# Kernel tuning notes

Measured on AMD Instinct MI355X. Metric: run time of the kernel, lower is better.

Reference implementation:

```python
import jax, jax.numpy as jnp
import numpy as np

B = 8          # batch size (static)
GRID = 1024    # spatial grid H = W
PER = 25000    # active sites per batch item
N = B * PER

_OFFSETS = [(dx, dy) for dx in (-1, 0, 1) for dy in (-1, 0, 1)]  # 3x3 kernel


def _build_sparse_inputs():
    """Sample unique active 2D coords per batch item and build the 3x3
    submanifold neighbor map: nbr[i, k] = index of neighbor site at kernel
    offset k, or -1 if that coordinate is inactive."""
    rng = np.random.default_rng(0)
    bs, xs, ys = [], [], []
    for b in range(B):
        flat = rng.choice(GRID * GRID, size=PER, replace=False)
        bs.append(np.full(PER, b, np.int64))
        xs.append((flat // GRID).astype(np.int64))
        ys.append((flat % GRID).astype(np.int64))
    bb = np.concatenate(bs); xx = np.concatenate(xs); yy = np.concatenate(ys)
    # hash lookup table: (b, x, y) -> site index
    lut = np.full(B * GRID * GRID, -1, np.int64)
    lut[bb * GRID * GRID + xx * GRID + yy] = np.arange(N, dtype=np.int64)
    nbr = np.full((N, 9), -1, np.int64)
    for k, (dx, dy) in enumerate(_OFFSETS):
        nx, ny = xx + dx, yy + dy
        ok = (nx >= 0) & (nx < GRID) & (ny >= 0) & (ny < GRID)
        key = bb * GRID * GRID + np.clip(nx, 0, GRID - 1) * GRID + np.clip(ny, 0, GRID - 1)
        nbr[:, k] = np.where(ok, lut[key], -1)
    return bb, nbr


def setup_inputs() -> dict:
    key = jax.random.key(0)
    k1, k2, k3 = jax.random.split(key, 3)
    batch_np, nbr_np = _build_sparse_inputs()
    feats = jax.random.normal(k1, (N, 3), dtype=jnp.float32)
    # He (kaiming normal, relu): std = sqrt(2 / fan_in), fan_in = 9 * Cin
    W1 = jax.random.normal(k2, (9, 3, 256), dtype=jnp.float32) * np.sqrt(2.0 / (9 * 3))
    W2 = jax.random.normal(k3, (9, 256, 256), dtype=jnp.float32) * np.sqrt(2.0 / (9 * 256))
    return {
        "feats": feats,
        "W1": W1,
        "W2": W2,
        "nbr": jnp.asarray(nbr_np),
        "batch_ids": jnp.asarray(batch_np),
    }


def _subm_conv(feat, W, nbr):
    """Submanifold 3x3 conv: out[i] = sum_k feat[nbr[i,k]] @ W[k] over valid
    neighbors. feat: [N, Cin], W: [9, Cin, Cout], nbr: [N, 9] -> [N, Cout]."""
    out = jnp.zeros((feat.shape[0], W.shape[2]), dtype=feat.dtype)
    for k in range(9):  # fixed small kernel loop
        idx = nbr[:, k]
        valid = (idx >= 0).astype(feat.dtype)[:, None]
        g = feat[jnp.maximum(idx, 0)] * valid  # masked gather [N, Cin]
        out = out + g @ W[k]
    return out


def reference(feats, W1, W2, nbr, batch_ids):
    h = jax.nn.relu(_subm_conv(feats, W1, nbr))   # [N, 256]
    h = jax.nn.relu(_subm_conv(h, W2, nbr))       # [N, 256]
    # global average pool per batch item -> [B, 256]
    sums = jax.ops.segment_sum(h, batch_ids, num_segments=B)
    counts = jax.ops.segment_sum(jnp.ones((h.shape[0],), h.dtype), batch_ids, num_segments=B)
    return sums / counts[:, None]
```

## Files before the change

### kernel.cpp

```cpp
#include <hip/hip_runtime.h>
#include <hip/hip_bf16.h>

typedef __attribute__((ext_vector_type(8))) short bh8;
typedef __attribute__((ext_vector_type(4))) float f32x4;

#define NB 8
#define SLOTS 64
#define CAP 6144
#define CROWS 36864
#define CGB 256
#define FROWS 64

__device__ __forceinline__ void gld_lds16(const void* g, void* l) {
  __builtin_amdgcn_global_load_lds(
      (const __attribute__((address_space(1))) void*)g,
      (__attribute__((address_space(3))) void*)l, 16, 0, 0);
}

__device__ __forceinline__ unsigned short f2bu(float f) {
  union { __hip_bfloat16 h; unsigned short u; } cv;
  cv.h = __float2bfloat16(f);
  return cv.u;
}
__device__ __forceinline__ float bu2f(unsigned short u) {
  return __uint_as_float(((unsigned)u) << 16);
}

__global__ __launch_bounds__(256, 2) void phase1_kernel(
    const float* __restrict__ feats, const float* __restrict__ W1,
    const float* __restrict__ W2, const int* __restrict__ nbr,
    const int* __restrict__ bid, __hip_bfloat16* __restrict__ h1b,
    __hip_bfloat16* __restrict__ w2bt, int* __restrict__ nOff,
    int* __restrict__ cnt, float* __restrict__ bcnt, int* __restrict__ cidmap,
    int* __restrict__ crow, int* __restrict__ psrc, int* __restrict__ pcnt_cid,
    int* __restrict__ pairlist, int N) {
  __shared__ union {
    struct { unsigned short w1s[256 * 32]; int s_nbr[64 * 9]; } c1;
    struct { int l_cnt[10]; int l_base[10]; int l_bcnt[NB]; } bld;
    struct { float tile[16][256]; } w2;
  } sm;

  const int nc1 = (N + 63) >> 6;
  const int nbld = (N + 255) >> 8;
  int bx = blockIdx.x;
  const int tid = threadIdx.x;

  if (bx < nc1) {
    const int base = bx * 64;
#pragma unroll 9
    for (int kk = 0; kk < 27; ++kk)
      sm.c1.w1s[tid * 32 + kk] = f2bu(W1[kk * 256 + tid]);
#pragma unroll
    for (int kk = 27; kk < 32; ++kk) sm.c1.w1s[tid * 32 + kk] = 0;
    for (int t = tid; t < 64 * 9; t += 256) sm.c1.s_nbr[t] = nbr[base * 9 + t];
    __syncthreads();

    const int wave = tid >> 6, lane = tid & 63;
    const int q = lane >> 4, m16 = lane & 15;
    const int rbase = (wave * 16 + m16) * 9;
    const int* s_nbr = sm.c1.s_nbr;

    float v[9 * 3];
    int t_lo[4] = {0, 2, 5, 8}, t_hi[4] = {3, 6, 8, 9};
    for (int tt = t_lo[q]; tt < t_hi[q]; ++tt) {
      int s = s_nbr[rbase + tt];
      long long sc = (s < 0) ? 0 : s;
      float x = feats[3 * sc], y = feats[3 * sc + 1], z = feats[3 * sc + 2];
      if (s < 0) { x = 0.f; y = 0.f; z = 0.f; }
      v[tt * 3 + 0] = x; v[tt * 3 + 1] = y; v[tt * 3 + 2] = z;
    }
    bh8 a;
#pragma unroll
    for (int j = 0; j < 8; ++j) {
      int col = q * 8 + j;
      a[j] = (col < 27) ? (short)f2bu(v[col]) : (short)0;
    }

    f32x4 acc[16];
#pragma unroll
    for (int nj = 0; nj < 16; ++nj) {
      bh8 b = *(const bh8*)(&sm.c1.w1s[(nj * 16 + m16) * 32 + q * 8]);
      acc[nj] = __builtin_amdgcn_mfma_f32_16x16x32_bf16(a, b, (f32x4)0.f, 0, 0, 0);
    }
    const int growb = base + wave * 16 + q * 4;
#pragma unroll
    for (int rr = 0; rr < 4; ++rr) {
      __hip_bfloat16* rowp = h1b + (long long)(growb + rr) * 256 + m16;
#pragma unroll
      for (int nj = 0; nj < 16; ++nj)
        rowp[nj * 16] = __float2bfloat16(fmaxf(acc[nj][rr], 0.f));
    }
    return;
  }
  bx -= nc1;

  if (bx < nbld) {
    if (tid < 10) sm.bld.l_cnt[tid] = 0;
    if (tid < NB) sm.bld.l_bcnt[tid] = 0;
    __syncthreads();

    const int i = bx * 256 + tid;
    const bool active = (i < N);
    int s[9];
    int kpos[9];
    int loc_cid = -1;
    if (active) {
#pragma unroll
      for (int k = 0; k < 9; ++k) s[k] = nbr[i * 9 + k];
      bool any = false;
#pragma unroll
      for (int k = 0; k < 9; ++k)
        if (k != 4 && s[k] >= 0) any = true;
      if (any) {
        loc_cid = atomicAdd(&sm.bld.l_cnt[9], 1);
#pragma unroll
        for (int k = 0; k < 9; ++k) {
          kpos[k] = -1;
          if (k != 4 && s[k] >= 0) kpos[k] = atomicAdd(&sm.bld.l_cnt[k], 1);
        }
      }
      atomicAdd(&sm.bld.l_bcnt[bid[i]], 1);
    }
    __syncthreads();

    if (tid < 9)
      sm.bld.l_base[tid] =
          (sm.bld.l_cnt[tid] > 0) ? atomicAdd(&cnt[tid], sm.bld.l_cnt[tid]) : 0;
    else if (tid == 9)
      sm.bld.l_base[9] = (sm.bld.l_cnt[9] > 0) ? atomicAdd(nOff, sm.bld.l_cnt[9]) : 0;
    if (tid >= 32 && tid < 32 + NB && sm.bld.l_bcnt[tid - 32] > 0)
      atomicAdd(&bcnt[tid - 32], (float)sm.bld.l_bcnt[tid - 32]);
    __syncthreads();

    if (active) {
      int cid = -1;
      if (loc_cid >= 0) {
        cid = sm.bld.l_base[9] + loc_cid;
        if (cid >= CROWS) cid = -1;
      }
      cidmap[i] = cid;
      if (cid >= 0) {
        crow[cid] = i;
#pragma unroll
        for (int k = 0; k < 9; ++k) {
          if (k == 4 || kpos[k] < 0 || s[k] < 0) continue;
          int pos = sm.bld.l_base[k] + kpos[k];
          if (pos < CAP) {
            psrc[k * CAP + pos] = s[k];
            int slot = atomicAdd(&pcnt_cid[cid], 1);
            if (slot < 8) pairlist[cid * 8 + slot] = k * CAP + pos;
          }
        }
      }
    }
    return;
  }
  bx -= nbld;

  {
    int k = bx >> 4, t = bx & 15;
#pragma unroll
    for (int r = 0; r < 16; ++r)
      sm.w2.tile[r][tid] = W2[k * 65536 + (t * 16 + r) * 256 + tid];
    __syncthreads();
#pragma unroll
    for (int r = 0; r < 16; ++r)
      w2bt[k * 65536 + tid * 256 + t * 16 + r] = __float2bfloat16(sm.w2.tile[r][tid]);
  }
}

__global__ __launch_bounds__(512, 2) void phase2_kernel(
    const __hip_bfloat16* __restrict__ h1, const __hip_bfloat16* __restrict__ w2bt,
    const int* __restrict__ cidmap, const int* __restrict__ bid,
    const int* __restrict__ cnt, const int* __restrict__ psrc,
    const int* __restrict__ nOffp, const int* __restrict__ crow,
    float* __restrict__ psums, unsigned short* __restrict__ h2cb,
    unsigned short* __restrict__ pout, int N) {
  __shared__ __align__(16) short Abuf[2][64 * 256];

  int bx = blockIdx.x;
  const int tid = threadIdx.x;
  const int wave = tid >> 6, lane = tid & 63;
  const int q = lane >> 4, m16 = lane & 15;
  const short* h1s = (const short*)h1;

  if (bx < CGB) {
    const int wc = wave << 5;
    const int slot = bx & (SLOTS - 1);
    const short* wts = (const short*)w2bt + 4 * 65536;

    bh8 breg[2][8];
#pragma unroll
    for (int nj = 0; nj < 2; ++nj)
#pragma unroll
      for (int ko = 0; ko < 8; ++ko)
        breg[nj][ko] =
            *(const bh8*)(wts + (wc + nj * 16 + m16) * 256 + ko * 32 + q * 8);

    const int nchunk = (N + 63) >> 6;
    const int span = (nchunk + CGB - 1) / CGB;
    const int c0 = bx * span;
    if (c0 >= nchunk) return;
    int c1 = c0 + span;
    if (c1 > nchunk) c1 = nchunk;

    const int lrow = lane >> 5;
    const int jch = lane & 31;

#define STAGE_CHUNK(cc, b)                                                     \
  {                                                                            \
    _Pragma("unroll") for (int t = 0; t < 4; ++t) {                            \
      int lr = (wave << 3) + (t << 1) + lrow;                                  \
      int g = ((cc) << 6) + lr;                                                \
      if (g >= N) g = N - 1;                                                   \
      int js = jch ^ (lr & 31);                                                \
      const short* src = h1s + (long long)g * 256 + (js << 3);                 \
      short* dst = &Abuf[b][((wave << 3) + (t << 1)) << 8];                    \
      gld_lds16((const void*)src, (void*)dst);                                 \
    }                                                                          \
  }

#define FLUSH_SACC()                                                           \
  if (cur_b0 >= 0) {                                                           \
    _Pragma("unroll") for (int lb = 0; lb < 2; ++lb) {                         \
      _Pragma("unroll") for (int nj = 0; nj < 2; ++nj) {                       \
        float v = sacc[lb][nj];                                                \
        v += __shfl_xor(v, 16, 64);                                            \
        v += __shfl_xor(v, 32, 64);                                            \
        if (q == 0 && v != 0.f) {                                              \
          int b = cur_b0 + lb;                                                 \
          if (b < NB)                                                          \
            atomicAdd(&psums[(slot * NB + b) * 256 + wc + nj * 16 + m16], v);  \
        }                                                                      \
      }                                                                        \
    }                                                                          \
  }

    STAGE_CHUNK(c0, 0);
    int cur = 0;
    int cur_b0 = -1;
    float sacc[2][2];
#pragma unroll
    for (int lb = 0; lb < 2; ++lb)
#pragma unroll
      for (int nj = 0; nj < 2; ++nj) sacc[lb][nj] = 0.f;

    for (int c = c0; c < c1; ++c) {
      __syncthreads();

      int4 bid4[4], cid4[4];
#pragma unroll
      for (int mi = 0; mi < 4; ++mi) {
        const int rb = (c << 6) + mi * 16 + q * 4;
        bid4[mi] = *(const int4*)(&bid[rb]);
        cid4[mi] = *(const int4*)(&cidmap[rb]);
      }
      const int b0 = bid[c << 6];

      if (c + 1 < c1) STAGE_CHUNK(c + 1, cur ^ 1);

      const short* Ab = &Abuf[cur][0];
      const short* abase[4];
      int xr[4];
#pragma unroll
      for (int mi = 0; mi < 4; ++mi) {
        int R = mi * 16 + m16;
        xr[mi] = R & 31;
        abase[mi] = Ab + (R << 8);
      }

      f32x4 acc[4][2];
#pragma unroll
      for (int ko = 0; ko < 8; ++ko) {
        bh8 a[4];
#pragma unroll
        for (int mi = 0; mi < 4; ++mi)
          a[mi] = *(const bh8*)(abase[mi] + (((ko * 4 + q) ^ xr[mi]) << 3));
#pragma unroll
        for (int mi = 0; mi < 4; ++mi)
#pragma unroll
          for (int nj = 0; nj < 2; ++nj)
            acc[mi][nj] = __builtin_amdgcn_mfma_f32_16x16x32_bf16(
                a[mi], breg[nj][ko], (ko == 0) ? (f32x4)0.f : acc[mi][nj], 0, 0, 0);
      }

      if (b0 != cur_b0) {
        FLUSH_SACC();
#pragma unroll
        for (int lb = 0; lb < 2; ++lb)
#pragma unroll
          for (int nj = 0; nj < 2; ++nj) sacc[lb][nj] = 0.f;
        cur_b0 = b0;
      }
#pragma unroll
      for (int mi = 0; mi < 4; ++mi) {
        const int bb[4] = {bid4[mi].x, bid4[mi].y, bid4[mi].z, bid4[mi].w};
        const int cc4[4] = {cid4[mi].x, cid4[mi].y, cid4[mi].z, cid4[mi].w};
        const int rb = (c << 6) + mi * 16 + q * 4;
#pragma unroll
        for (int rr = 0; rr < 4; ++rr) {
          if (rb + rr >= N) continue;
          if (cc4[rr] >= 0) continue;
          const int lb = (bb[rr] != b0) ? 1 : 0;
#pragma unroll
          for (int nj = 0; nj < 2; ++nj)
            sacc[lb][nj] += fmaxf(acc[mi][nj][rr], 0.f);
        }
      }
      cur ^= 1;
    }
    FLUSH_SACC();
#undef STAGE_CHUNK
#undef FLUSH_SACC
    return;
  }
  bx -= CGB;

  int* s_src = (int*)&Abuf[0][0];
  const int OFFG = 8 * (CAP / 64);
  int k = 4;
  int gbase, cmax;
  bool isoff;
  if (bx < OFFG) {
    int koff = bx / (CAP / 64);
    int grp = bx - koff * (CAP / 64);
    k = koff + (koff >= 4 ? 1 : 0);
    cmax = cnt[k];
    gbase = grp * 64;
    isoff = true;
  } else {
    bx -= OFFG;
    cmax = *nOffp;
    if (cmax > CROWS) cmax = CROWS;
    gbase = bx * 64;
    isoff = false;
  }
  if (gbase >= cmax) return;

  if (tid < 64) {
    int m = gbase + tid;
    s_src[tid] = (m < cmax) ? (isoff ? psrc[k * CAP + m] : crow[m]) : 0;
  }
  const short* wts = (const short*)w2bt + k * 65536;
  const int wc = wave << 5;

  bh8 breg[2][8];
#pragma unroll
  for (int nj = 0; nj < 2; ++nj)
#pragma unroll
    for (int ko = 0; ko < 8; ++ko)
      breg[nj][ko] = *(const bh8*)(wts + (wc + nj * 16 + m16) * 256 + ko * 32 + q * 8);
  __syncthreads();

  for (int t = 0; t < 4; ++t) {
    if (gbase + t * 16 >= cmax) break;
    bh8 aA[8];
    {
      const short* ap = h1s + (long long)s_src[t * 16 + m16] * 256 + q * 8;
#pragma unroll
      for (int ko = 0; ko < 8; ++ko) aA[ko] = *(const bh8*)(ap + ko * 32);
    }
    f32x4 acc[2];
#pragma unroll
    for (int ko = 0; ko < 8; ++ko)
#pragma unroll
      for (int nj = 0; nj < 2; ++nj)
        acc[nj] = __builtin_amdgcn_mfma_f32_16x16x32_bf16(
            aA[ko], breg[nj][ko], (ko == 0) ? (f32x4)0.f : acc[nj], 0, 0, 0);
#pragma unroll
    for (int r = 0; r < 4; ++r) {
      int m = gbase + t * 16 + q * 4 + r;
      if (m >= cmax) continue;
      unsigned short* dst =
          isoff ? (pout + (long long)(k * CAP + m) * 256) : (h2cb + (long long)m * 256);
      dst[wc + m16] = f2bu(acc[0][r]);
      dst[wc + 16 + m16] = f2bu(acc[1][r]);
    }
  }
}

__global__ __launch_bounds__(256) void fixup_kernel(
    const unsigned short* __restrict__ h2cb, const unsigned short* __restrict__ pout,
    const int* __restrict__ pairlist, const int* __restrict__ pcnt_cid,
    const int* __restrict__ crow, const int* __restrict__ bid,
    const int* __restrict__ nOffp, float* __restrict__ psums) {
  __shared__ float lsum[NB * 256];
  __shared__ int s_b[FROWS], s_np[FROWS], s_pl[FROWS * 8];
  int nc = *nOffp;
  if (nc > CROWS) nc = CROWS;
  const int t0 = blockIdx.x * FROWS;
  if (t0 >= nc) return;
  const int tid = threadIdx.x;

  if (tid < FROWS) {
    int m = t0 + tid;
    bool v = (m < nc);
    s_b[tid] = v ? bid[crow[m]] : -1;
    int np = v ? pcnt_cid[m] : 0;
    s_np[tid] = (np > 8) ? 8 : np;
  }
  for (int i = tid; i < FROWS * 8; i += 256) {
    int m = t0 + (i >> 3);
    s_pl[i] = (m < nc) ? pairlist[m * 8 + (i & 7)] : 0;
  }
#pragma unroll
  for (int b = 0; b < NB; ++b) lsum[b * 256 + tid] = 0.f;
  __syncthreads();

  const int g = tid >> 6;
  const int cg = tid & 63;
  const ushort4* h2v = (const ushort4*)h2cb;
  const ushort4* pov = (const ushort4*)pout;

  float4 s0 = {0.f, 0.f, 0.f, 0.f}, s1 = {0.f, 0.f, 0.f, 0.f};
  const int r0 = g * 16;
  const int b0 = s_b[r0];
  int b1 = -1;
  for (int r = r0; r < r0 + 16; ++r) {
    const int b = s_b[r];
    if (b < 0) break;
    ushort4 u = h2v[(long long)(t0 + r) * 64 + cg];
    float4 x = {bu2f(u.x), bu2f(u.y), bu2f(u.z), bu2f(u.w)};
    const int np = s_np[r];
    for (int j = 0; j < np; ++j) {
      ushort4 p = pov[(long long)s_pl[r * 8 + j] * 64 + cg];
      x.x += bu2f(p.x); x.y += bu2f(p.y); x.z += bu2f(p.z); x.w += bu2f(p.w);
    }
    x.x = fmaxf(x.x, 0.f); x.y = fmaxf(x.y, 0.f);
    x.z = fmaxf(x.z, 0.f); x.w = fmaxf(x.w, 0.f);
    if (b == b0) {
      s0.x += x.x; s0.y += x.y; s0.z += x.z; s0.w += x.w;
    } else {
      b1 = b;
      s1.x += x.x; s1.y += x.y; s1.z += x.z; s1.w += x.w;
    }
  }
  if (b0 >= 0) {
    float* p0 = &lsum[b0 * 256 + cg * 4];
    atomicAdd(p0 + 0, s0.x); atomicAdd(p0 + 1, s0.y);
    atomicAdd(p0 + 2, s0.z); atomicAdd(p0 + 3, s0.w);
  }
  if (b1 >= 0 && b1 < NB) {
    float* p1 = &lsum[b1 * 256 + cg * 4];
    atomicAdd(p1 + 0, s1.x); atomicAdd(p1 + 1, s1.y);
    atomicAdd(p1 + 2, s1.z); atomicAdd(p1 + 3, s1.w);
  }
  __syncthreads();

  const int slot = blockIdx.x & (SLOTS - 1);
#pragma unroll
  for (int b = 0; b < NB; ++b) {
    float v = lsum[b * 256 + tid];
    if (v != 0.f) atomicAdd(&psums[(slot * NB + b) * 256 + tid], v);
  }
}

__global__ void finalize_kernel(const float* __restrict__ psums,
                                const float* __restrict__ bcnt,
                                float* __restrict__ out) {
  int b = blockIdx.x, c = threadIdx.x;
  float s = 0.f;
  for (int t = 0; t < SLOTS; ++t) s += psums[(t * NB + b) * 256 + c];
  out[b * 256 + c] = s / bcnt[b];
}

extern "C" void kernel_launch(void* const* d_in, const int* in_sizes, int n_in,
                              void* d_out, int out_size, void* d_ws, size_t ws_size,
                              hipStream_t stream) {
  const float* feats = (const float*)d_in[0];
  const float* W1    = (const float*)d_in[1];
  const float* W2    = (const float*)d_in[2];
  const int*   nbr   = (const int*)d_in[3];
  const int*   bid   = (const int*)d_in[4];
  float* out = (float*)d_out;
  const int N = in_sizes[0] / 3;

  char* ws = (char*)d_ws;
  size_t o = 0;
  float* psums = (float*)(ws + o); o += (size_t)SLOTS * NB * 256 * 4;
  float* bcnt  = (float*)(ws + o); o += NB * 4;
  int*   nOff  = (int*)(ws + o);   o += 4;
  int*   cnt   = (int*)(ws + o);   o += 9 * 4;
  o = (o + 255) & ~(size_t)255;
  int* pcnt_cid = (int*)(ws + o); o += (size_t)CROWS * 4;
  size_t zero1 = o;
  int* psrc = (int*)(ws + o); o += (size_t)9 * CAP * 4;
  int* pairlist = (int*)(ws + o); o += (size_t)CROWS * 8 * 4;
  int* cidmap = (int*)(ws + o); o += (size_t)N * 4;
  int* crow = (int*)(ws + o); o += (size_t)CROWS * 4;
  o = (o + 255) & ~(size_t)255;
  unsigned short* h2cb = (unsigned short*)(ws + o); o += (size_t)CROWS * 256 * 2;
  unsigned short* pout = (unsigned short*)(ws + o); o += (size_t)9 * CAP * 256 * 2;
  __hip_bfloat16* w2bt = (__hip_bfloat16*)(ws + o); o += (size_t)9 * 65536 * 2;
  __hip_bfloat16* h1b  = (__hip_bfloat16*)(ws + o); o += (size_t)N * 256 * 2;

  hipMemsetAsync(d_ws, 0, zero1, stream);

  const int nc1 = (N + 63) / 64;
  const int nbld = (N + 255) / 256;
  phase1_kernel<<<nc1 + nbld + 144, 256, 0, stream>>>(
      feats, W1, W2, nbr, bid, h1b, w2bt, nOff, cnt, bcnt, cidmap, crow, psrc,
      pcnt_cid, pairlist, N);
  phase2_kernel<<<CGB + 8 * (CAP / 64) + CROWS / 64, 512, 0, stream>>>(
      h1b, w2bt, cidmap, bid, cnt, psrc, nOff, crow, psums, h2cb, pout, N);
  fixup_kernel<<<(CROWS + FROWS - 1) / FROWS, 256, 0, stream>>>(
      h2cb, pout, pairlist, pcnt_cid, crow, bid, nOff, psums);
  finalize_kernel<<<NB, 256, 0, stream>>>(psums, bcnt, out);
}
```

Before: 272.1 us.

## Split phase2 into separate off-center and center GEMM kernels with prefetching

The merged phase2 kernel is split into two launches. One is an off-center/center-row gather GEMM kernel with 256 threads, where each wave covers 64 output columns and the next 16-row A tile is prefetched into registers. The other is a dedicated center-tap GEMM kernel that keeps the LDS double-buffered pipeline. The phase1 feature gather is also unrolled into explicit per-quarter branches to avoid a dynamic-indexed register array. The goal is to cut register/LDS pressure for the off-center blocks and give each kernel its own occupancy. The cost is an extra launch boundary and serialization between the two GEMMs.

```diff
diff --git a/kernel.cpp b/kernel.cpp
--- a/kernel.cpp
+++ b/kernel.cpp
@@ -8,7 +8,7 @@
 #define SLOTS 64
 #define CAP 6144
 #define CROWS 36864
-#define CGB 256
+#define CBLOCKS 256
 #define FROWS 64
 
 __device__ __forceinline__ void gld_lds16(const void* g, void* l) {
@@ -24,6 +24,16 @@
 }
 __device__ __forceinline__ float bu2f(unsigned short u) {
   return __uint_as_float(((unsigned)u) << 16);
+}
+
+__device__ __forceinline__ float3 ldf3(const float* __restrict__ f,
+                                       const int* s_nbr, int idx) {
+  int s = s_nbr[idx];
+  long long sc = (s < 0) ? 0 : s;
+  float3 r;
+  r.x = f[3 * sc]; r.y = f[3 * sc + 1]; r.z = f[3 * sc + 2];
+  if (s < 0) { r.x = 0.f; r.y = 0.f; r.z = 0.f; }
+  return r;
 }
 
 __global__ __launch_bounds__(256, 2) void phase1_kernel(
@@ -60,20 +70,34 @@
     const int rbase = (wave * 16 + m16) * 9;
     const int* s_nbr = sm.c1.s_nbr;
 
-    float v[9 * 3];
-    int t_lo[4] = {0, 2, 5, 8}, t_hi[4] = {3, 6, 8, 9};
-    for (int tt = t_lo[q]; tt < t_hi[q]; ++tt) {
-      int s = s_nbr[rbase + tt];
-      long long sc = (s < 0) ? 0 : s;
-      float x = feats[3 * sc], y = feats[3 * sc + 1], z = feats[3 * sc + 2];
-      if (s < 0) { x = 0.f; y = 0.f; z = 0.f; }
-      v[tt * 3 + 0] = x; v[tt * 3 + 1] = y; v[tt * 3 + 2] = z;
-    }
     bh8 a;
-#pragma unroll
-    for (int j = 0; j < 8; ++j) {
-      int col = q * 8 + j;
-      a[j] = (col < 27) ? (short)f2bu(v[col]) : (short)0;
+    if (q == 0) {
+      float3 t0 = ldf3(feats, s_nbr, rbase + 0);
+      float3 t1 = ldf3(feats, s_nbr, rbase + 1);
+      float3 t2 = ldf3(feats, s_nbr, rbase + 2);
+      a[0] = (short)f2bu(t0.x); a[1] = (short)f2bu(t0.y); a[2] = (short)f2bu(t0.z);
+      a[3] = (short)f2bu(t1.x); a[4] = (short)f2bu(t1.y); a[5] = (short)f2bu(t1.z);
+      a[6] = (short)f2bu(t2.x); a[7] = (short)f2bu(t2.y);
+    } else if (q == 1) {
+      float3 t2 = ldf3(feats, s_nbr, rbase + 2);
+      float3 t3 = ldf3(feats, s_nbr, rbase + 3);
+      float3 t4 = ldf3(feats, s_nbr, rbase + 4);
+      float3 t5 = ldf3(feats, s_nbr, rbase + 5);
+      a[0] = (short)f2bu(t2.z);
+      a[1] = (short)f2bu(t3.x); a[2] = (short)f2bu(t3.y); a[3] = (short)f2bu(t3.z);
+      a[4] = (short)f2bu(t4.x); a[5] = (short)f2bu(t4.y); a[6] = (short)f2bu(t4.z);
+      a[7] = (short)f2bu(t5.x);
+    } else if (q == 2) {
+      float3 t5 = ldf3(feats, s_nbr, rbase + 5);
+      float3 t6 = ldf3(feats, s_nbr, rbase + 6);
+      float3 t7 = ldf3(feats, s_nbr, rbase + 7);
+      a[0] = (short)f2bu(t5.y); a[1] = (short)f2bu(t5.z);
+      a[2] = (short)f2bu(t6.x); a[3] = (short)f2bu(t6.y); a[4] = (short)f2bu(t6.z);
+      a[5] = (short)f2bu(t7.x); a[6] = (short)f2bu(t7.y); a[7] = (short)f2bu(t7.z);
+    } else {
+      float3 t8 = ldf3(feats, s_nbr, rbase + 8);
+      a[0] = (short)f2bu(t8.x); a[1] = (short)f2bu(t8.y); a[2] = (short)f2bu(t8.z);
+      a[3] = 0; a[4] = 0; a[5] = 0; a[6] = 0; a[7] = 0;
     }
 
     f32x4 acc[16];
@@ -169,43 +193,37 @@
   }
 }
 
-__global__ __launch_bounds__(512, 2) void phase2_kernel(
+__global__ __launch_bounds__(512, 2) void center_gemm_kernel(
     const __hip_bfloat16* __restrict__ h1, const __hip_bfloat16* __restrict__ w2bt,
     const int* __restrict__ cidmap, const int* __restrict__ bid,
-    const int* __restrict__ cnt, const int* __restrict__ psrc,
-    const int* __restrict__ nOffp, const int* __restrict__ crow,
-    float* __restrict__ psums, unsigned short* __restrict__ h2cb,
-    unsigned short* __restrict__ pout, int N) {
+    float* __restrict__ psums, int N) {
   __shared__ __align__(16) short Abuf[2][64 * 256];
 
-  int bx = blockIdx.x;
   const int tid = threadIdx.x;
   const int wave = tid >> 6, lane = tid & 63;
   const int q = lane >> 4, m16 = lane & 15;
+  const int wc = wave << 5;
+  const int slot = blockIdx.x & (SLOTS - 1);
+
   const short* h1s = (const short*)h1;
-
-  if (bx < CGB) {
-    const int wc = wave << 5;
-    const int slot = bx & (SLOTS - 1);
-    const short* wts = (const short*)w2bt + 4 * 65536;
-
-    bh8 breg[2][8];
-#pragma unroll
-    for (int nj = 0; nj < 2; ++nj)
-#pragma unroll
-      for (int ko = 0; ko < 8; ++ko)
-        breg[nj][ko] =
-            *(const bh8*)(wts + (wc + nj * 16 + m16) * 256 + ko * 32 + q * 8);
-
-    const int nchunk = (N + 63) >> 6;
-    const int span = (nchunk + CGB - 1) / CGB;
-    const int c0 = bx * span;
-    if (c0 >= nchunk) return;
-    int c1 = c0 + span;
-    if (c1 > nchunk) c1 = nchunk;
-
-    const int lrow = lane >> 5;
-    const int jch = lane & 31;
+  const short* wts = (const short*)w2bt + 4 * 65536;
+
+  bh8 breg[2][8];
+#pragma unroll
+  for (int nj = 0; nj < 2; ++nj)
+#pragma unroll
+    for (int ko = 0; ko < 8; ++ko)
+      breg[nj][ko] = *(const bh8*)(wts + (wc + nj * 16 + m16) * 256 + ko * 32 + q * 8);
+
+  const int nchunk = (N + 63) >> 6;
+  const int span = (nchunk + CBLOCKS - 1) / CBLOCKS;
+  const int c0 = blockIdx.x * span;
+  if (c0 >= nchunk) return;
+  int c1 = c0 + span;
+  if (c1 > nchunk) c1 = nchunk;
+
+  const int lrow = lane >> 5;
+  const int jch = lane & 31;
 
 #define STAGE_CHUNK(cc, b)                                                     \
   {                                                                            \
@@ -236,100 +254,104 @@
     }                                                                          \
   }
 
-    STAGE_CHUNK(c0, 0);
-    int cur = 0;
-    int cur_b0 = -1;
-    float sacc[2][2];
-#pragma unroll
-    for (int lb = 0; lb < 2; ++lb)
-#pragma unroll
-      for (int nj = 0; nj < 2; ++nj) sacc[lb][nj] = 0.f;
-
-    for (int c = c0; c < c1; ++c) {
-      __syncthreads();
-
-      int4 bid4[4], cid4[4];
-#pragma unroll
-      for (int mi = 0; mi < 4; ++mi) {
-        const int rb = (c << 6) + mi * 16 + q * 4;
-        bid4[mi] = *(const int4*)(&bid[rb]);
-        cid4[mi] = *(const int4*)(&cidmap[rb]);
+  STAGE_CHUNK(c0, 0);
+  int cur = 0;
+  int cur_b0 = -1;
+  float sacc[2][2];
+#pragma unroll
+  for (int lb = 0; lb < 2; ++lb)
+#pragma unroll
+    for (int nj = 0; nj < 2; ++nj) sacc[lb][nj] = 0.f;
+
+  for (int c = c0; c < c1; ++c) {
+    __syncthreads();
+
+    int4 bid4[4], cid4[4];
+#pragma unroll
+    for (int mi = 0; mi < 4; ++mi) {
+      const int rb = (c << 6) + mi * 16 + q * 4;
+      bid4[mi] = *(const int4*)(&bid[rb]);
+      cid4[mi] = *(const int4*)(&cidmap[rb]);
+    }
+    const int b0 = bid[c << 6];
+
+    if (c + 1 < c1) STAGE_CHUNK(c + 1, cur ^ 1);
+
+    const short* Ab = &Abuf[cur][0];
+    const short* abase[4];
+    int xr[4];
+#pragma unroll
+    for (int mi = 0; mi < 4; ++mi) {
+      int R = mi * 16 + m16;
+      xr[mi] = R & 31;
+      abase[mi] = Ab + (R << 8);
+    }
+
+    f32x4 acc[4][2];
+#pragma unroll
+    for (int ko = 0; ko < 8; ++ko) {
+      bh8 a[4];
+#pragma unroll
+      for (int mi = 0; mi < 4; ++mi)
+        a[mi] = *(const bh8*)(abase[mi] + (((ko * 4 + q) ^ xr[mi]) << 3));
+#pragma unroll
+      for (int mi = 0; mi < 4; ++mi)
+#pragma unroll
+        for (int nj = 0; nj < 2; ++nj)
+          acc[mi][nj] = __builtin_amdgcn_mfma_f32_16x16x32_bf16(
+              a[mi], breg[nj][ko], (ko == 0) ? (f32x4)0.f : acc[mi][nj], 0, 0, 0);
+    }
+
+    if (b0 != cur_b0) {
+      FLUSH_SACC();
+#pragma unroll
+      for (int lb = 0; lb < 2; ++lb)
+#pragma unroll
+        for (int nj = 0; nj < 2; ++nj) sacc[lb][nj] = 0.f;
+      cur_b0 = b0;
+    }
+#pragma unroll
+    for (int mi = 0; mi < 4; ++mi) {
+      const int bb[4] = {bid4[mi].x, bid4[mi].y, bid4[mi].z, bid4[mi].w};
+      const int cc4[4] = {cid4[mi].x, cid4[mi].y, cid4[mi].z, cid4[mi].w};
+      const int rb = (c << 6) + mi * 16 + q * 4;
+#pragma unroll
+      for (int rr = 0; rr < 4; ++rr) {
+        if (rb + rr >= N) continue;
+        if (cc4[rr] >= 0) continue;
+        const int lb = (bb[rr] != b0) ? 1 : 0;
+#pragma unroll
+        for (int nj = 0; nj < 2; ++nj)
+          sacc[lb][nj] += fmaxf(acc[mi][nj][rr], 0.f);
       }
-      const int b0 = bid[c << 6];
-
-      if (c + 1 < c1) STAGE_CHUNK(c + 1, cur ^ 1);
-
-      const short* Ab = &Abuf[cur][0];
-      const short* abase[4];
-      int xr[4];
-#pragma unroll
-      for (int mi = 0; mi < 4; ++mi) {
-        int R = mi * 16 + m16;
-        xr[mi] = R & 31;
-        abase[mi] = Ab + (R << 8);
-      }
-
-      f32x4 acc[4][2];
-#pragma unroll
-      for (int ko = 0; ko < 8; ++ko) {
-        bh8 a[4];
-#pragma unroll
-        for (int mi = 0; mi < 4; ++mi)
-          a[mi] = *(const bh8*)(abase[mi] + (((ko * 4 + q) ^ xr[mi]) << 3));
-#pragma unroll
-        for (int mi = 0; mi < 4; ++mi)
-#pragma unroll
-          for (int nj = 0; nj < 2; ++nj)
-            acc[mi][nj] = __builtin_amdgcn_mfma_f32_16x16x32_bf16(
-                a[mi], breg[nj][ko], (ko == 0) ? (f32x4)0.f : acc[mi][nj], 0, 0, 0);
-      }
-
-      if (b0 != cur_b0) {
-        FLUSH_SACC();
-#pragma unroll
-        for (int lb = 0; lb < 2; ++lb)
-#pragma unroll
-          for (int nj = 0; nj < 2; ++nj) sacc[lb][nj] = 0.f;
-        cur_b0 = b0;
-      }
-#pragma unroll
-      for (int mi = 0; mi < 4; ++mi) {
-        const int bb[4] = {bid4[mi].x, bid4[mi].y, bid4[mi].z, bid4[mi].w};
-        const int cc4[4] = {cid4[mi].x, cid4[mi].y, cid4[mi].z, cid4[mi].w};
-        const int rb = (c << 6) + mi * 16 + q * 4;
-#pragma unroll
-        for (int rr = 0; rr < 4; ++rr) {
-          if (rb + rr >= N) continue;
-          if (cc4[rr] >= 0) continue;
-          const int lb = (bb[rr] != b0) ? 1 : 0;
-#pragma unroll
-          for (int nj = 0; nj < 2; ++nj)
-            sacc[lb][nj] += fmaxf(acc[mi][nj][rr], 0.f);
-        }
-      }
-      cur ^= 1;
-    }
-    FLUSH_SACC();
+    }
+    cur ^= 1;
+  }
+  FLUSH_SACC();
 #undef STAGE_CHUNK
 #undef FLUSH_SACC
-    return;
-  }
-  bx -= CGB;
-
-  int* s_src = (int*)&Abuf[0][0];
-  const int OFFG = 8 * (CAP / 64);
-  int k = 4;
-  int gbase, cmax;
+}
+
+__global__ __launch_bounds__(256, 2) void offctap_kernel(
+    const __hip_bfloat16* __restrict__ h1, const __hip_bfloat16* __restrict__ w2bt,
+    const int* __restrict__ cnt, const int* __restrict__ psrc,
+    const int* __restrict__ nOffp, const int* __restrict__ crow,
+    unsigned short* __restrict__ pout, unsigned short* __restrict__ h2cb) {
+  const int bpk = CAP / 64;
+  const int OFFG = 8 * bpk;
+  int bx = blockIdx.x;
+  int k, gbase, cmax;
   bool isoff;
   if (bx < OFFG) {
-    int koff = bx / (CAP / 64);
-    int grp = bx - koff * (CAP / 64);
+    int koff = bx / bpk;
+    int grp = bx - koff * bpk;
     k = koff + (koff >= 4 ? 1 : 0);
     cmax = cnt[k];
     gbase = grp * 64;
     isoff = true;
   } else {
     bx -= OFFG;
+    k = 4;
     cmax = *nOffp;
     if (cmax > CROWS) cmax = CROWS;
     gbase = bx * 64;
@@ -337,45 +359,60 @@
   }
   if (gbase >= cmax) return;
 
+  __shared__ int s_src[64];
+  const int tid = threadIdx.x;
   if (tid < 64) {
     int m = gbase + tid;
     s_src[tid] = (m < cmax) ? (isoff ? psrc[k * CAP + m] : crow[m]) : 0;
   }
+
+  const int wave = tid >> 6, lane = tid & 63, q = lane >> 4, m16 = lane & 15;
+  const short* h1s = (const short*)h1;
   const short* wts = (const short*)w2bt + k * 65536;
-  const int wc = wave << 5;
-
-  bh8 breg[2][8];
-#pragma unroll
-  for (int nj = 0; nj < 2; ++nj)
+
+  bh8 breg[4][8];
+#pragma unroll
+  for (int nj = 0; nj < 4; ++nj)
 #pragma unroll
     for (int ko = 0; ko < 8; ++ko)
-      breg[nj][ko] = *(const bh8*)(wts + (wc + nj * 16 + m16) * 256 + ko * 32 + q * 8);
+      breg[nj][ko] = *(const bh8*)(wts + (wave * 64 + nj * 16 + m16) * 256 + ko * 32 + q * 8);
   __syncthreads();
 
+  bh8 aA[8];
+  {
+    const short* ap = h1s + (long long)s_src[m16] * 256 + q * 8;
+#pragma unroll
+    for (int ko = 0; ko < 8; ++ko) aA[ko] = *(const bh8*)(ap + ko * 32);
+  }
+
+#pragma unroll
   for (int t = 0; t < 4; ++t) {
-    if (gbase + t * 16 >= cmax) break;
-    bh8 aA[8];
-    {
-      const short* ap = h1s + (long long)s_src[t * 16 + m16] * 256 + q * 8;
-#pragma unroll
-      for (int ko = 0; ko < 8; ++ko) aA[ko] = *(const bh8*)(ap + ko * 32);
-    }
-    f32x4 acc[2];
+    bh8 aN[8];
+    if (t < 3) {
+      const short* ap = h1s + (long long)s_src[(t + 1) * 16 + m16] * 256 + q * 8;
+#pragma unroll
+      for (int ko = 0; ko < 8; ++ko) aN[ko] = *(const bh8*)(ap + ko * 32);
+    }
+    f32x4 acc[4];
 #pragma unroll
     for (int ko = 0; ko < 8; ++ko)
 #pragma unroll
-      for (int nj = 0; nj < 2; ++nj)
+      for (int nj = 0; nj < 4; ++nj)
         acc[nj] = __builtin_amdgcn_mfma_f32_16x16x32_bf16(
             aA[ko], breg[nj][ko], (ko == 0) ? (f32x4)0.f : acc[nj], 0, 0, 0);
 #pragma unroll
     for (int r = 0; r < 4; ++r) {
       int m = gbase + t * 16 + q * 4 + r;
       if (m >= cmax) continue;
-      unsigned short* dst =
-          isoff ? (pout + (long long)(k * CAP + m) * 256) : (h2cb + (long long)m * 256);
-      dst[wc + m16] = f2bu(acc[0][r]);
-      dst[wc + 16 + m16] = f2bu(acc[1][r]);
-    }
+      unsigned short* dst = isoff ? (pout + (long long)(k * CAP + m) * 256)
+                                  : (h2cb + (long long)m * 256);
+#pragma unroll
+      for (int nj = 0; nj < 4; ++nj)
+        dst[wave * 64 + nj * 16 + m16] = f2bu(acc[nj][r]);
+    }
+#pragma unroll
+    for (int ko = 0; ko < 8; ++ko) aA[ko] = aN[ko];
+    if (gbase + (t + 1) * 16 >= cmax) break;
   }
 }
 
@@ -501,8 +538,9 @@
   phase1_kernel<<<nc1 + nbld + 144, 256, 0, stream>>>(
       feats, W1, W2, nbr, bid, h1b, w2bt, nOff, cnt, bcnt, cidmap, crow, psrc,
       pcnt_cid, pairlist, N);
-  phase2_kernel<<<CGB + 8 * (CAP / 64) + CROWS / 64, 512, 0, stream>>>(
-      h1b, w2bt, cidmap, bid, cnt, psrc, nOff, crow, psums, h2cb, pout, N);
+  offctap_kernel<<<8 * (CAP / 64) + CROWS / 64, 256, 0, stream>>>(
+      h1b, w2bt, cnt, psrc, nOff, crow, pout, h2cb);
+  center_gemm_kernel<<<CBLOCKS, 512, 0, stream>>>(h1b, w2bt, cidmap, bid, psums, N);
   fixup_kernel<<<(CROWS + FROWS - 1) / FROWS, 256, 0, stream>>>(
       h2cb, pout, pairlist, pcnt_cid, crow, bid, nOff, psums);
   finalize_kernel<<<NB, 256, 0, stream>>>(psums, bcnt, out);
```

New measurement: 248.9 us. 1.09x faster.
